# Kernel optimization log

Hardware: AMD Instinct MI355X
Metric: run time of the kernel (lower is better)

## Reference

```python
import jax, jax.numpy as jnp
import numpy as np

N_NODES = 50000
EPS = 1e-5


def sage_conv_max(x, src, dst, W_l, b_l, W_r):
    # PyG SAGEConv(aggr='max'): out = lin_l(max_j x_j) + lin_r(x_i)
    msg = x[src]                                   # [E, d] gather
    agg = jnp.full((x.shape[0], x.shape[1]), -jnp.inf, dtype=x.dtype)
    agg = agg.at[dst].max(msg)                     # scatter-max over edges
    agg = jnp.where(jnp.isneginf(agg), 0.0, agg)   # isolated nodes -> 0 (PyG convention)
    return agg @ W_l.T + b_l + x @ W_r.T


def batch_norm(x, gamma, beta):
    mean = jnp.mean(x, axis=0)
    var = jnp.var(x, axis=0)
    return (x - mean) * jax.lax.rsqrt(var + EPS) * gamma + beta


def setup_inputs() -> dict:
    key = jax.random.key(0)
    ks = jax.random.split(key, 10)
    d_in, d_h, d_out = 128, 128, 32
    s = lambda fan: 1.0 / np.sqrt(fan)
    return {
        "x": jax.random.normal(ks[0], (N_NODES, d_in), dtype=jnp.float32),
        "edge_index": jax.random.randint(ks[1], (2, 800000), 0, N_NODES, dtype=jnp.int32),
        "W_l1": jax.random.uniform(ks[2], (d_h, d_in), jnp.float32, -s(d_in), s(d_in)),
        "b_l1": jnp.zeros((d_h,), jnp.float32),
        "W_r1": jax.random.uniform(ks[3], (d_h, d_in), jnp.float32, -s(d_in), s(d_in)),
        "gamma1": jnp.ones((d_h,), jnp.float32),
        "beta1": jnp.zeros((d_h,), jnp.float32),
        "W_l2": jax.random.uniform(ks[4], (d_out, d_h), jnp.float32, -s(d_h), s(d_h)),
        "b_l2": jnp.zeros((d_out,), jnp.float32),
        "W_r2": jax.random.uniform(ks[5], (d_out, d_h), jnp.float32, -s(d_h), s(d_h)),
    }


def reference(x, edge_index, W_l1, b_l1, W_r1, gamma1, beta1, W_l2, b_l2, W_r2):
    src, dst = edge_index[0], edge_index[1]
    h = sage_conv_max(x, src, dst, W_l1, b_l1, W_r1)
    h = batch_norm(h, gamma1, beta1)
    h = jax.nn.relu(h)
    # dropout is identity at inference
    return sage_conv_max(h, src, dst, W_l2, b_l2, W_r2)
```

## Files before the change

### kernel.cpp

```cpp
#include <hip/hip_runtime.h>
#include <math.h>
#include <float.h>

#define N_NODES 50000
#define N_EDGES 800000
#define NB 392
#define EB 2048
#define NBUCK 196
#define BSH 8
#define CAP 36
#define SEGC 4864
#define CELLS_PER_BUCKET (NB * CAP)

typedef __attribute__((ext_vector_type(8))) short bf16x8;
typedef __attribute__((ext_vector_type(4))) float f32x4;

static __device__ __forceinline__ unsigned short f2bf(float f) {
  unsigned int u = __float_as_uint(f);
  u = (u + 0x7fff + ((u >> 16) & 1)) >> 16;
  return (unsigned short)u;
}

__global__ __launch_bounds__(256) void setup_kernel(
    const int* __restrict__ src, const int* __restrict__ dst,
    unsigned int* __restrict__ pairs, int* __restrict__ counts,
    const float* __restrict__ x, const float* __restrict__ Wl1,
    const float* __restrict__ Wr1, const float* __restrict__ Wl2,
    const float* __restrict__ Wr2, unsigned int* __restrict__ x_bf,
    unsigned short* __restrict__ Wcat1, unsigned short* __restrict__ Wcat2,
    float* __restrict__ gsums) {
  const int b = blockIdx.x, tid = threadIdx.x;
  if (b < NB) {
    __shared__ int cur[NBUCK];
    if (tid < NBUCK) cur[tid] = 0;
    __syncthreads();
#pragma unroll
    for (int it = 0; it < EB / 256; ++it) {
      int e = b * EB + it * 256 + tid;
      if (e < N_EDGES) {
        int d = dst[e];
        int bk = d >> BSH;
        int p = atomicAdd(&cur[bk], 1);
        if (p < CAP)
          pairs[(size_t)(bk * NB + b) * CAP + p] =
              (unsigned)src[e] | ((unsigned)(d & 255) << 16);
      }
    }
    __syncthreads();
    if (tid < NBUCK) {
      int c = cur[tid];
      counts[tid * NB + b] = c > CAP ? CAP : c;
    }
  } else if (b < NB + 6250) {
    int i = (b - NB) * 256 + tid;
    float4 v = ((const float4*)x)[i];
    uint2 o;
    o.x = (unsigned int)f2bf(v.x) | ((unsigned int)f2bf(v.y) << 16);
    o.y = (unsigned int)f2bf(v.z) | ((unsigned int)f2bf(v.w) << 16);
    ((uint2*)x_bf)[i] = o;
  } else if (b < NB + 6410) {
    int i = (b - NB - 6250) * 256 + tid;
    if (i < 32768) {
      int n = i >> 8, k = i & 255;
      float w = (k < 128) ? Wl1[n * 128 + k] : Wr1[n * 128 + (k - 128)];
      Wcat1[i] = f2bf(w);
    } else if (i < 40960) {
      int j = i - 32768;
      int n = j >> 8, k = j & 255;
      float w = (k < 128) ? Wl2[n * 128 + k] : Wr2[n * 128 + (k - 128)];
      Wcat2[j] = f2bf(w);
    }
  } else {
#pragma unroll
    for (int i = 0; i < 8; ++i) gsums[i * 256 + tid] = 0.f;
  }
}

__global__ __launch_bounds__(1024) void bucket_sort(const unsigned int* __restrict__ pairs,
                                                    const int* __restrict__ counts,
                                                    unsigned int* __restrict__ rowinfo,
                                                    int* __restrict__ elist) {
  __shared__ int hist[256], cpos[256], cnt[NB];
  __shared__ int wsum[4];
  const int b = blockIdx.x, tid = threadIdx.x;
  const size_t s0 = (size_t)b * CELLS_PER_BUCKET;
  if (tid < 256) hist[tid] = 0;
  if (tid < NB) cnt[tid] = counts[b * NB + tid];
  __syncthreads();
  for (int p = tid; p < CELLS_PER_BUCKET; p += 1024) {
    int c = p / CAP, s = p - c * CAP;
    if (s < cnt[c]) {
      unsigned int pr = pairs[s0 + p];
      atomicAdd(&hist[(pr >> 16) & 255], 1);
    }
  }
  __syncthreads();
  int incl = 0, h = 0;
  if (tid < 256) {
    const int l = tid & 63;
    h = hist[tid];
    incl = h;
#pragma unroll
    for (int off = 1; off < 64; off <<= 1) {
      int t = __shfl_up(incl, off, 64);
      if (l >= off) incl += t;
    }
    if (l == 63) wsum[tid >> 6] = incl;
  }
  __syncthreads();
  if (tid < 64) {
    int v = (tid < 4) ? wsum[tid] : 0;
#pragma unroll
    for (int off = 1; off < 4; off <<= 1) {
      int t = __shfl_up(v, off, 64);
      if (tid >= off) v += t;
    }
    if (tid < 4) wsum[tid] = v;
  }
  __syncthreads();
  if (tid < 256) {
    const int w = tid >> 6;
    int tot = incl + ((w > 0) ? wsum[w - 1] : 0);
    int excl = tot - h;
    cpos[tid] = excl;
    int node = (b << BSH) + tid;
    if (node < N_NODES)
      rowinfo[node] = (unsigned)(b * SEGC + excl) | ((unsigned)h << 20);
  }
  __syncthreads();
  for (int p = tid; p < CELLS_PER_BUCKET; p += 1024) {
    int c = p / CAP, s = p - c * CAP;
    if (s < cnt[c]) {
      unsigned int pr = pairs[s0 + p];
      int loc = atomicAdd(&cpos[(pr >> 16) & 255], 1);
      elist[b * SEGC + loc] = (int)(pr & 0xffffu);
    }
  }
}

template <bool BN>
__global__ __launch_bounds__(256) void agg_max_bf16(const uint4* __restrict__ feat4,
                                                    const unsigned int* __restrict__ rowinfo,
                                                    const int* __restrict__ elist,
                                                    const float* __restrict__ gsums,
                                                    const float* __restrict__ gamma,
                                                    const float* __restrict__ beta,
                                                    uint4* __restrict__ out4) {
  __shared__ float s_scale[128], s_shift[128];
  if (BN) {
    int t = threadIdx.x;
    if (t < 128) {
      float sm = 0.f, sq = 0.f;
#pragma unroll
      for (int r = 0; r < 8; ++r) {
        sm += gsums[r * 256 + t];
        sq += gsums[r * 256 + 128 + t];
      }
      const float inv = 1.f / (float)N_NODES;
      float mean = sm * inv;
      float var = sq * inv - mean * mean;
      float sc = gamma[t] * rsqrtf(var + 1e-5f);
      s_scale[t] = sc;
      s_shift[t] = beta[t] - mean * sc;
    }
    __syncthreads();
  }

  int node = blockIdx.x * 4 + (threadIdx.x >> 6);
  int lane = threadIdx.x & 63;
  int eslot = lane >> 4;
  int fq = lane & 15;
  unsigned int info = rowinfo[node];
  int e0 = (int)(info & 0xFFFFFu);
  int deg = (int)(info >> 20);
  int e1 = e0 + deg;
  float m[8];
#pragma unroll
  for (int j = 0; j < 8; ++j) m[j] = -FLT_MAX;

  if (deg > 0) {
    const int last = e1 - 1;
    for (int base = e0; base < e1; base += 16) {
      int idx[4];
#pragma unroll
      for (int q = 0; q < 4; ++q) {
        int e = base + q * 4 + eslot;
        if (e > last) e = last;
        idx[q] = elist[e];
      }
      uint4 v[4];
#pragma unroll
      for (int q = 0; q < 4; ++q) v[q] = feat4[(size_t)idx[q] * 16 + fq];
#pragma unroll
      for (int q = 0; q < 4; ++q) {
        const unsigned int* pv = (const unsigned int*)&v[q];
#pragma unroll
        for (int c = 0; c < 4; ++c) {
          m[2 * c]     = fmaxf(m[2 * c],     __uint_as_float(pv[c] << 16));
          m[2 * c + 1] = fmaxf(m[2 * c + 1], __uint_as_float(pv[c] & 0xffff0000u));
        }
      }
    }
  }

#pragma unroll
  for (int j = 0; j < 8; ++j) {
    m[j] = fmaxf(m[j], __shfl_xor(m[j], 16, 64));
    m[j] = fmaxf(m[j], __shfl_xor(m[j], 32, 64));
  }
  if (eslot == 0) {
    if (deg == 0) {
#pragma unroll
      for (int j = 0; j < 8; ++j) m[j] = 0.f;
    } else if (BN) {
#pragma unroll
      for (int j = 0; j < 8; ++j) {
        int col = fq * 8 + j;
        m[j] = fmaxf(m[j] * s_scale[col] + s_shift[col], 0.f);
      }
    }
    uint4 o;
    o.x = (unsigned)f2bf(m[0]) | ((unsigned)f2bf(m[1]) << 16);
    o.y = (unsigned)f2bf(m[2]) | ((unsigned)f2bf(m[3]) << 16);
    o.z = (unsigned)f2bf(m[4]) | ((unsigned)f2bf(m[5]) << 16);
    o.w = (unsigned)f2bf(m[6]) | ((unsigned)f2bf(m[7]) << 16);
    out4[(size_t)node * 16 + fq] = o;
  }
}

#define ASTR 264

template <int NT, bool BF16OUT, bool STATS, bool BNIN>
__global__ __launch_bounds__(256) void gemm_mfma(
    const unsigned short* __restrict__ Aa, const unsigned short* __restrict__ Ab,
    const unsigned short* __restrict__ Wcat, const float* __restrict__ bias,
    unsigned short* __restrict__ outb, float* __restrict__ outf,
    float* __restrict__ gsums, const float* __restrict__ gamma,
    const float* __restrict__ beta, int N) {
  __shared__ unsigned short Alds[128 * ASTR];
  __shared__ float s_sum[128], s_sq[128];
  __shared__ float s_scale[128], s_shift[128];
  const int tid = threadIdx.x;
  const int rowBase = blockIdx.x * 128;

  if (STATS && tid < 128) { s_sum[tid] = 0.f; s_sq[tid] = 0.f; }
  if (BNIN) {
    if (tid < 128) {
      float sm = 0.f, sq = 0.f;
#pragma unroll
      for (int r = 0; r < 8; ++r) {
        sm += gsums[r * 256 + tid];
        sq += gsums[r * 256 + 128 + tid];
      }
      const float inv = 1.f / (float)N_NODES;
      float mean = sm * inv;
      float var = sq * inv - mean * mean;
      float sc = gamma[tid] * rsqrtf(var + 1e-5f);
      s_scale[tid] = sc;
      s_shift[tid] = beta[tid] - mean * sc;
    }
    __syncthreads();
  }

#pragma unroll
  for (int it = 0; it < 16; ++it) {
    int f = tid + it * 256;
    int r = f >> 5;
    int seg = f & 31;
    int n = rowBase + r;
    if (n >= N) n = N - 1;
    const unsigned short* src = (seg < 16)
        ? (Aa + (size_t)n * 128 + seg * 8)
        : (Ab + (size_t)n * 128 + (seg - 16) * 8);
    int4 d = *(const int4*)src;
    if (BNIN && seg >= 16) {
      int kb = (seg - 16) * 8;
      unsigned int* dp = (unsigned int*)&d;
#pragma unroll
      for (int c = 0; c < 4; ++c) {
        int k0 = kb + 2 * c;
        float lo = __uint_as_float(dp[c] << 16);
        float hi = __uint_as_float(dp[c] & 0xffff0000u);
        lo = fmaxf(lo * s_scale[k0] + s_shift[k0], 0.f);
        hi = fmaxf(hi * s_scale[k0 + 1] + s_shift[k0 + 1], 0.f);
        dp[c] = (unsigned)f2bf(lo) | ((unsigned)f2bf(hi) << 16);
      }
    }
    *(int4*)(&Alds[r * ASTR + seg * 8]) = d;
  }
  __syncthreads();

  const int wv = tid >> 6;
  const int lane = tid & 63;
  const int ln15 = lane & 15;
  const int quad = lane >> 4;
  const int m0 = wv * 32;

  f32x4 acc[2][NT] = {};

#pragma unroll
  for (int ks = 0; ks < 8; ++ks) {
    const int k0 = ks * 32;
    bf16x8 a0 = *(const bf16x8*)(&Alds[(m0 + ln15) * ASTR + k0 + quad * 8]);
    bf16x8 a1 = *(const bf16x8*)(&Alds[(m0 + 16 + ln15) * ASTR + k0 + quad * 8]);
#pragma unroll
    for (int nt = 0; nt < NT; ++nt) {
      bf16x8 b = *(const bf16x8*)(Wcat + (size_t)(nt * 16 + ln15) * 256 + k0 + quad * 8);
      acc[0][nt] = __builtin_amdgcn_mfma_f32_16x16x32_bf16(a0, b, acc[0][nt], 0, 0, 0);
      acc[1][nt] = __builtin_amdgcn_mfma_f32_16x16x32_bf16(a1, b, acc[1][nt], 0, 0, 0);
    }
  }

  const int ldo = NT * 16;
#pragma unroll
  for (int nt = 0; nt < NT; ++nt) {
    int col = nt * 16 + ln15;
    float bv = bias[col];
    float psum = 0.f, psq = 0.f;
#pragma unroll
    for (int mt = 0; mt < 2; ++mt) {
#pragma unroll
      for (int i = 0; i < 4; ++i) {
        int r = rowBase + m0 + mt * 16 + quad * 4 + i;
        if (r < N) {
          float val = acc[mt][nt][i] + bv;
          if (STATS) { psum += val; psq += val * val; }
          if (BF16OUT)
            outb[(size_t)r * ldo + col] = f2bf(val);
          else
            outf[(size_t)r * ldo + col] = val;
        }
      }
    }
    if (STATS) {
      atomicAdd(&s_sum[col], psum);
      atomicAdd(&s_sq[col], psq);
    }
  }
  if (STATS) {
    __syncthreads();
    if (tid < 128) {
      int rep = blockIdx.x & 7;
      atomicAdd(&gsums[rep * 256 + tid], s_sum[tid]);
      atomicAdd(&gsums[rep * 256 + 128 + tid], s_sq[tid]);
    }
  }
}

extern "C" void kernel_launch(void* const* d_in, const int* in_sizes, int n_in,
                              void* d_out, int out_size, void* d_ws, size_t ws_size,
                              hipStream_t stream) {
  (void)in_sizes; (void)n_in; (void)out_size; (void)ws_size;
  const float* x     = (const float*)d_in[0];
  const int*   eidx  = (const int*)d_in[1];
  const float* W_l1  = (const float*)d_in[2];
  const float* b_l1  = (const float*)d_in[3];
  const float* W_r1  = (const float*)d_in[4];
  const float* gamma = (const float*)d_in[5];
  const float* beta  = (const float*)d_in[6];
  const float* W_l2  = (const float*)d_in[7];
  const float* b_l2  = (const float*)d_in[8];
  const float* W_r2  = (const float*)d_in[9];
  const int* srcp = eidx;
  const int* dstp = eidx + N_EDGES;
  float* out = (float*)d_out;

  int* wsi = (int*)d_ws;
  float* gsums   = (float*)wsi;
  unsigned int* rowinfo = (unsigned int*)(wsi + 2048);
  int*   counts  = wsi + 52224;
  int*   elist   = wsi + 129056;
  unsigned int* pairs   = (unsigned int*)(wsi + 1082400);
  unsigned int* x_bf    = (unsigned int*)(wsi + 3848352);
  unsigned int* agg_bf  = (unsigned int*)(wsi + 7048352);
  unsigned int* h_bf    = (unsigned int*)(wsi + 10248352);
  unsigned short* Wcat1 = (unsigned short*)(wsi + 13448352);
  unsigned short* Wcat2 = (unsigned short*)(wsi + 13464736);

  setup_kernel<<<dim3(NB + 6410 + 1), 256, 0, stream>>>(
      srcp, dstp, pairs, counts, x, W_l1, W_r1, W_l2, W_r2, x_bf, Wcat1, Wcat2, gsums);

  bucket_sort<<<dim3(NBUCK), 1024, 0, stream>>>(pairs, counts, rowinfo, elist);

  agg_max_bf16<false><<<dim3(N_NODES / 4), 256, 0, stream>>>(
      (const uint4*)x_bf, rowinfo, elist, nullptr, nullptr, nullptr, (uint4*)agg_bf);
  gemm_mfma<8, true, true, false><<<dim3(391), 256, 0, stream>>>(
      (const unsigned short*)agg_bf, (const unsigned short*)x_bf, Wcat1, b_l1,
      (unsigned short*)h_bf, nullptr, gsums, nullptr, nullptr, N_NODES);

  agg_max_bf16<true><<<dim3(N_NODES / 4), 256, 0, stream>>>(
      (const uint4*)h_bf, rowinfo, elist, gsums, gamma, beta, (uint4*)agg_bf);
  gemm_mfma<2, false, false, true><<<dim3(391), 256, 0, stream>>>(
      (const unsigned short*)agg_bf, (const unsigned short*)h_bf, Wcat2, b_l2,
      nullptr, out, gsums, gamma, beta, N_NODES);
}
```

Before: 215.7 us.

## Split max-aggregation into feature slices and fold conversions into sort kernel

The gather-max kernel now processes one 32-feature slice per block across four slice passes. Each thread loads one 4-byte word per edge instead of 16 bytes, so each pass touches a smaller feature window, which is meant to improve cache locality on random neighbor gathers. The edge scatter is moved into its own kernel, and the x/weight bf16 conversions and gsums zeroing are moved from it into the bucket-sort launch so they run alongside the sort. The cost is more blocks, narrower loads, and repeated elist and rowinfo reads for every slice.

```diff
diff --git a/kernel.cpp b/kernel.cpp
--- a/kernel.cpp
+++ b/kernel.cpp
@@ -3,6 +3,7 @@
 #include <float.h>
 
 #define N_NODES 50000
+#define N_PAD 50176
 #define N_EDGES 800000
 #define NB 392
 #define EB 2048
@@ -11,6 +12,9 @@
 #define CAP 36
 #define SEGC 4864
 #define CELLS_PER_BUCKET (NB * CAP)
+#define GB (N_PAD / 4)
+#define XC_BLKS 1563
+#define WC_BLKS 40
 
 typedef __attribute__((ext_vector_type(8))) short bf16x8;
 typedef __attribute__((ext_vector_type(4))) float f32x4;
@@ -21,68 +25,71 @@
   return (unsigned short)u;
 }
 
-__global__ __launch_bounds__(256) void setup_kernel(
+__global__ __launch_bounds__(512) void scatter_kernel(
     const int* __restrict__ src, const int* __restrict__ dst,
-    unsigned int* __restrict__ pairs, int* __restrict__ counts,
+    unsigned int* __restrict__ pairs, int* __restrict__ counts) {
+  const int b = blockIdx.x, tid = threadIdx.x;
+  __shared__ int cur[NBUCK];
+  if (tid < NBUCK) cur[tid] = 0;
+  __syncthreads();
+#pragma unroll
+  for (int it = 0; it < EB / 512; ++it) {
+    int e = b * EB + it * 512 + tid;
+    if (e < N_EDGES) {
+      int d = dst[e];
+      int bk = d >> BSH;
+      int p = atomicAdd(&cur[bk], 1);
+      if (p < CAP)
+        pairs[(size_t)(bk * NB + b) * CAP + p] =
+            (unsigned)src[e] | ((unsigned)(d & 255) << 16);
+    }
+  }
+  __syncthreads();
+  if (tid < NBUCK) {
+    int c = cur[tid];
+    counts[tid * NB + b] = c > CAP ? CAP : c;
+  }
+}
+
+__global__ __launch_bounds__(1024) void sort_conv_kernel(
+    const unsigned int* __restrict__ pairs, const int* __restrict__ counts,
+    unsigned int* __restrict__ rowinfo, int* __restrict__ elist,
     const float* __restrict__ x, const float* __restrict__ Wl1,
     const float* __restrict__ Wr1, const float* __restrict__ Wl2,
     const float* __restrict__ Wr2, unsigned int* __restrict__ x_bf,
     unsigned short* __restrict__ Wcat1, unsigned short* __restrict__ Wcat2,
     float* __restrict__ gsums) {
   const int b = blockIdx.x, tid = threadIdx.x;
-  if (b < NB) {
-    __shared__ int cur[NBUCK];
-    if (tid < NBUCK) cur[tid] = 0;
-    __syncthreads();
-#pragma unroll
-    for (int it = 0; it < EB / 256; ++it) {
-      int e = b * EB + it * 256 + tid;
-      if (e < N_EDGES) {
-        int d = dst[e];
-        int bk = d >> BSH;
-        int p = atomicAdd(&cur[bk], 1);
-        if (p < CAP)
-          pairs[(size_t)(bk * NB + b) * CAP + p] =
-              (unsigned)src[e] | ((unsigned)(d & 255) << 16);
-      }
-    }
-    __syncthreads();
-    if (tid < NBUCK) {
-      int c = cur[tid];
-      counts[tid * NB + b] = c > CAP ? CAP : c;
-    }
-  } else if (b < NB + 6250) {
-    int i = (b - NB) * 256 + tid;
-    float4 v = ((const float4*)x)[i];
-    uint2 o;
-    o.x = (unsigned int)f2bf(v.x) | ((unsigned int)f2bf(v.y) << 16);
-    o.y = (unsigned int)f2bf(v.z) | ((unsigned int)f2bf(v.w) << 16);
-    ((uint2*)x_bf)[i] = o;
-  } else if (b < NB + 6410) {
-    int i = (b - NB - 6250) * 256 + tid;
-    if (i < 32768) {
-      int n = i >> 8, k = i & 255;
-      float w = (k < 128) ? Wl1[n * 128 + k] : Wr1[n * 128 + (k - 128)];
-      Wcat1[i] = f2bf(w);
-    } else if (i < 40960) {
-      int j = i - 32768;
-      int n = j >> 8, k = j & 255;
-      float w = (k < 128) ? Wl2[n * 128 + k] : Wr2[n * 128 + (k - 128)];
-      Wcat2[j] = f2bf(w);
-    }
-  } else {
-#pragma unroll
-    for (int i = 0; i < 8; ++i) gsums[i * 256 + tid] = 0.f;
-  }
-}
-
-__global__ __launch_bounds__(1024) void bucket_sort(const unsigned int* __restrict__ pairs,
-                                                    const int* __restrict__ counts,
-                                                    unsigned int* __restrict__ rowinfo,
-                                                    int* __restrict__ elist) {
+  if (b >= NBUCK) {
+    if (b < NBUCK + XC_BLKS) {
+      int i = (b - NBUCK) * 1024 + tid;
+      if (i < 1600000) {
+        float4 v = ((const float4*)x)[i];
+        uint2 o;
+        o.x = (unsigned int)f2bf(v.x) | ((unsigned int)f2bf(v.y) << 16);
+        o.y = (unsigned int)f2bf(v.z) | ((unsigned int)f2bf(v.w) << 16);
+        ((uint2*)x_bf)[i] = o;
+      }
+    } else if (b < NBUCK + XC_BLKS + WC_BLKS) {
+      int i = (b - NBUCK - XC_BLKS) * 1024 + tid;
+      if (i < 32768) {
+        int n = i >> 8, k = i & 255;
+        float w = (k < 128) ? Wl1[n * 128 + k] : Wr1[n * 128 + (k - 128)];
+        Wcat1[i] = f2bf(w);
+      } else if (i < 40960) {
+        int j = i - 32768;
+        int n = j >> 8, k = j & 255;
+        float w = (k < 128) ? Wl2[n * 128 + k] : Wr2[n * 128 + (k - 128)];
+        Wcat2[j] = f2bf(w);
+      }
+    } else {
+      gsums[tid] = 0.f;
+      gsums[tid + 1024] = 0.f;
+    }
+    return;
+  }
   __shared__ int hist[256], cpos[256], cnt[NB];
   __shared__ int wsum[4];
-  const int b = blockIdx.x, tid = threadIdx.x;
   const size_t s0 = (size_t)b * CELLS_PER_BUCKET;
   if (tid < 256) hist[tid] = 0;
   if (tid < NB) cnt[tid] = counts[b * NB + tid];
@@ -139,92 +146,80 @@
 }
 
 template <bool BN>
-__global__ __launch_bounds__(256) void agg_max_bf16(const uint4* __restrict__ feat4,
-                                                    const unsigned int* __restrict__ rowinfo,
-                                                    const int* __restrict__ elist,
-                                                    const float* __restrict__ gsums,
-                                                    const float* __restrict__ gamma,
-                                                    const float* __restrict__ beta,
-                                                    uint4* __restrict__ out4) {
-  __shared__ float s_scale[128], s_shift[128];
+__global__ __launch_bounds__(256) void gather_slice(
+    const unsigned int* __restrict__ feat,
+    const unsigned int* __restrict__ rowinfo,
+    const int* __restrict__ elist,
+    const float* __restrict__ gsums,
+    const float* __restrict__ gamma, const float* __restrict__ beta,
+    unsigned int* __restrict__ out) {
+  __shared__ float s_scale[32], s_shift[32];
+  const int bid = blockIdx.x;
+  const int slice = bid / GB;
+  const int nb = bid - slice * GB;
+  const int tid = threadIdx.x;
   if (BN) {
-    int t = threadIdx.x;
-    if (t < 128) {
+    if (tid < 32) {
+      int f = slice * 32 + tid;
       float sm = 0.f, sq = 0.f;
 #pragma unroll
       for (int r = 0; r < 8; ++r) {
-        sm += gsums[r * 256 + t];
-        sq += gsums[r * 256 + 128 + t];
+        sm += gsums[r * 256 + f];
+        sq += gsums[r * 256 + 128 + f];
       }
       const float inv = 1.f / (float)N_NODES;
       float mean = sm * inv;
       float var = sq * inv - mean * mean;
-      float sc = gamma[t] * rsqrtf(var + 1e-5f);
-      s_scale[t] = sc;
-      s_shift[t] = beta[t] - mean * sc;
+      float sc = gamma[f] * rsqrtf(var + 1e-5f);
+      s_scale[tid] = sc;
+      s_shift[tid] = beta[f] - mean * sc;
     }
     __syncthreads();
   }
-
-  int node = blockIdx.x * 4 + (threadIdx.x >> 6);
-  int lane = threadIdx.x & 63;
-  int eslot = lane >> 4;
-  int fq = lane & 15;
+  int node = nb * 4 + (tid >> 6);
+  if (node >= N_NODES) node = N_NODES - 1;
+  const int lane = tid & 63;
+  const int eslot = lane >> 4;
+  const int fq = lane & 15;
   unsigned int info = rowinfo[node];
   int e0 = (int)(info & 0xFFFFFu);
   int deg = (int)(info >> 20);
   int e1 = e0 + deg;
-  float m[8];
-#pragma unroll
-  for (int j = 0; j < 8; ++j) m[j] = -FLT_MAX;
-
+  float m0 = -FLT_MAX, m1 = -FLT_MAX;
+  const unsigned int* fs = feat + slice * 16 + fq;
   if (deg > 0) {
     const int last = e1 - 1;
-    for (int base = e0; base < e1; base += 16) {
-      int idx[4];
-#pragma unroll
-      for (int q = 0; q < 4; ++q) {
+    for (int base = e0; base < e1; base += 8) {
+      int idx[2];
+#pragma unroll
+      for (int q = 0; q < 2; ++q) {
         int e = base + q * 4 + eslot;
         if (e > last) e = last;
         idx[q] = elist[e];
       }
-      uint4 v[4];
-#pragma unroll
-      for (int q = 0; q < 4; ++q) v[q] = feat4[(size_t)idx[q] * 16 + fq];
-#pragma unroll
-      for (int q = 0; q < 4; ++q) {
-        const unsigned int* pv = (const unsigned int*)&v[q];
-#pragma unroll
-        for (int c = 0; c < 4; ++c) {
-          m[2 * c]     = fmaxf(m[2 * c],     __uint_as_float(pv[c] << 16));
-          m[2 * c + 1] = fmaxf(m[2 * c + 1], __uint_as_float(pv[c] & 0xffff0000u));
-        }
-      }
-    }
-  }
-
-#pragma unroll
-  for (int j = 0; j < 8; ++j) {
-    m[j] = fmaxf(m[j], __shfl_xor(m[j], 16, 64));
-    m[j] = fmaxf(m[j], __shfl_xor(m[j], 32, 64));
-  }
+      unsigned int v[2];
+#pragma unroll
+      for (int q = 0; q < 2; ++q) v[q] = fs[(size_t)idx[q] * 64];
+#pragma unroll
+      for (int q = 0; q < 2; ++q) {
+        m0 = fmaxf(m0, __uint_as_float(v[q] << 16));
+        m1 = fmaxf(m1, __uint_as_float(v[q] & 0xffff0000u));
+      }
+    }
+  }
+  m0 = fmaxf(m0, __shfl_xor(m0, 16, 64));
+  m0 = fmaxf(m0, __shfl_xor(m0, 32, 64));
+  m1 = fmaxf(m1, __shfl_xor(m1, 16, 64));
+  m1 = fmaxf(m1, __shfl_xor(m1, 32, 64));
   if (eslot == 0) {
     if (deg == 0) {
-#pragma unroll
-      for (int j = 0; j < 8; ++j) m[j] = 0.f;
+      m0 = 0.f; m1 = 0.f;
     } else if (BN) {
-#pragma unroll
-      for (int j = 0; j < 8; ++j) {
-        int col = fq * 8 + j;
-        m[j] = fmaxf(m[j] * s_scale[col] + s_shift[col], 0.f);
-      }
-    }
-    uint4 o;
-    o.x = (unsigned)f2bf(m[0]) | ((unsigned)f2bf(m[1]) << 16);
-    o.y = (unsigned)f2bf(m[2]) | ((unsigned)f2bf(m[3]) << 16);
-    o.z = (unsigned)f2bf(m[4]) | ((unsigned)f2bf(m[5]) << 16);
-    o.w = (unsigned)f2bf(m[6]) | ((unsigned)f2bf(m[7]) << 16);
-    out4[(size_t)node * 16 + fq] = o;
+      m0 = fmaxf(m0 * s_scale[2 * fq] + s_shift[2 * fq], 0.f);
+      m1 = fmaxf(m1 * s_scale[2 * fq + 1] + s_shift[2 * fq + 1], 0.f);
+    }
+    out[(size_t)node * 64 + slice * 16 + fq] =
+        (unsigned)f2bf(m0) | ((unsigned)f2bf(m1) << 16);
   }
 }
 
@@ -377,19 +372,20 @@
   unsigned short* Wcat1 = (unsigned short*)(wsi + 13448352);
   unsigned short* Wcat2 = (unsigned short*)(wsi + 13464736);
 
-  setup_kernel<<<dim3(NB + 6410 + 1), 256, 0, stream>>>(
-      srcp, dstp, pairs, counts, x, W_l1, W_r1, W_l2, W_r2, x_bf, Wcat1, Wcat2, gsums);
-
-  bucket_sort<<<dim3(NBUCK), 1024, 0, stream>>>(pairs, counts, rowinfo, elist);
-
-  agg_max_bf16<false><<<dim3(N_NODES / 4), 256, 0, stream>>>(
-      (const uint4*)x_bf, rowinfo, elist, nullptr, nullptr, nullptr, (uint4*)agg_bf);
+  scatter_kernel<<<dim3(NB), 512, 0, stream>>>(srcp, dstp, pairs, counts);
+
+  sort_conv_kernel<<<dim3(NBUCK + XC_BLKS + WC_BLKS + 1), 1024, 0, stream>>>(
+      pairs, counts, rowinfo, elist, x, W_l1, W_r1, W_l2, W_r2,
+      x_bf, Wcat1, Wcat2, gsums);
+
+  gather_slice<false><<<dim3(4 * GB), 256, 0, stream>>>(
+      x_bf, rowinfo, elist, nullptr, nullptr, nullptr, agg_bf);
   gemm_mfma<8, true, true, false><<<dim3(391), 256, 0, stream>>>(
       (const unsigned short*)agg_bf, (const unsigned short*)x_bf, Wcat1, b_l1,
       (unsigned short*)h_bf, nullptr, gsums, nullptr, nullptr, N_NODES);
 
-  agg_max_bf16<true><<<dim3(N_NODES / 4), 256, 0, stream>>>(
-      (const uint4*)h_bf, rowinfo, elist, gsums, gamma, beta, (uint4*)agg_bf);
+  gather_slice<true><<<dim3(4 * GB), 256, 0, stream>>>(
+      h_bf, rowinfo, elist, gsums, gamma, beta, agg_bf);
   gemm_mfma<2, false, false, true><<<dim3(391), 256, 0, stream>>>(
       (const unsigned short*)agg_bf, (const unsigned short*)h_bf, Wcat2, b_l2,
       nullptr, out, gsums, gamma, beta, N_NODES);
```

Measured after the change: 304.5 us. 41.1% more time.

## Load GEMM A operands directly from global, drop LDS staging and halve row tile

Applied to the files above, without the earlier changes.

The GEMM kernels no longer stage the 128-row A tile in LDS. Each wave now loads its 16-row A fragments straight from global memory, with BN+ReLU applied in registers for the second layer. The block covers 64 rows instead of 128 and the grid doubles to 784 blocks, which frees the large LDS allocation, raises occupancy and removes the staging sync. In exchange, each B fragment is reused across only one M tile instead of two, and the global A loads are strided per lane rather than fully coalesced.

```diff
diff --git a/kernel.cpp b/kernel.cpp
--- a/kernel.cpp
+++ b/kernel.cpp
@@ -228,8 +228,6 @@
   }
 }
 
-#define ASTR 264
-
 template <int NT, bool BF16OUT, bool STATS, bool BNIN>
 __global__ __launch_bounds__(256) void gemm_mfma(
     const unsigned short* __restrict__ Aa, const unsigned short* __restrict__ Ab,
@@ -237,56 +235,25 @@
     unsigned short* __restrict__ outb, float* __restrict__ outf,
     float* __restrict__ gsums, const float* __restrict__ gamma,
     const float* __restrict__ beta, int N) {
-  __shared__ unsigned short Alds[128 * ASTR];
   __shared__ float s_sum[128], s_sq[128];
   __shared__ float s_scale[128], s_shift[128];
   const int tid = threadIdx.x;
-  const int rowBase = blockIdx.x * 128;
+  const int rowBase = blockIdx.x * 64;
 
   if (STATS && tid < 128) { s_sum[tid] = 0.f; s_sq[tid] = 0.f; }
-  if (BNIN) {
-    if (tid < 128) {
-      float sm = 0.f, sq = 0.f;
-#pragma unroll
-      for (int r = 0; r < 8; ++r) {
-        sm += gsums[r * 256 + tid];
-        sq += gsums[r * 256 + 128 + tid];
-      }
-      const float inv = 1.f / (float)N_NODES;
-      float mean = sm * inv;
-      float var = sq * inv - mean * mean;
-      float sc = gamma[tid] * rsqrtf(var + 1e-5f);
-      s_scale[tid] = sc;
-      s_shift[tid] = beta[tid] - mean * sc;
-    }
-    __syncthreads();
-  }
-
-#pragma unroll
-  for (int it = 0; it < 16; ++it) {
-    int f = tid + it * 256;
-    int r = f >> 5;
-    int seg = f & 31;
-    int n = rowBase + r;
-    if (n >= N) n = N - 1;
-    const unsigned short* src = (seg < 16)
-        ? (Aa + (size_t)n * 128 + seg * 8)
-        : (Ab + (size_t)n * 128 + (seg - 16) * 8);
-    int4 d = *(const int4*)src;
-    if (BNIN && seg >= 16) {
-      int kb = (seg - 16) * 8;
-      unsigned int* dp = (unsigned int*)&d;
-#pragma unroll
-      for (int c = 0; c < 4; ++c) {
-        int k0 = kb + 2 * c;
-        float lo = __uint_as_float(dp[c] << 16);
-        float hi = __uint_as_float(dp[c] & 0xffff0000u);
-        lo = fmaxf(lo * s_scale[k0] + s_shift[k0], 0.f);
-        hi = fmaxf(hi * s_scale[k0 + 1] + s_shift[k0 + 1], 0.f);
-        dp[c] = (unsigned)f2bf(lo) | ((unsigned)f2bf(hi) << 16);
-      }
-    }
-    *(int4*)(&Alds[r * ASTR + seg * 8]) = d;
+  if (BNIN && tid < 128) {
+    float sm = 0.f, sq = 0.f;
+#pragma unroll
+    for (int r = 0; r < 8; ++r) {
+      sm += gsums[r * 256 + tid];
+      sq += gsums[r * 256 + 128 + tid];
+    }
+    const float inv = 1.f / (float)N_NODES;
+    float mean = sm * inv;
+    float var = sq * inv - mean * mean;
+    float sc = gamma[tid] * rsqrtf(var + 1e-5f);
+    s_scale[tid] = sc;
+    s_shift[tid] = beta[tid] - mean * sc;
   }
   __syncthreads();
 
@@ -294,20 +261,38 @@
   const int lane = tid & 63;
   const int ln15 = lane & 15;
   const int quad = lane >> 4;
-  const int m0 = wv * 32;
-
-  f32x4 acc[2][NT] = {};
+  const int mrow = rowBase + wv * 16;
+  int r0 = mrow + ln15;
+  if (r0 >= N) r0 = N - 1;
+
+  f32x4 acc[NT] = {};
 
 #pragma unroll
   for (int ks = 0; ks < 8; ++ks) {
-    const int k0 = ks * 32;
-    bf16x8 a0 = *(const bf16x8*)(&Alds[(m0 + ln15) * ASTR + k0 + quad * 8]);
-    bf16x8 a1 = *(const bf16x8*)(&Alds[(m0 + 16 + ln15) * ASTR + k0 + quad * 8]);
+    const int off = ks * 32 + quad * 8;
+    bf16x8 a;
+    if (ks < 4) {
+      a = *(const bf16x8*)(Aa + (size_t)r0 * 128 + off);
+    } else {
+      const int kb = off - 128;
+      a = *(const bf16x8*)(Ab + (size_t)r0 * 128 + kb);
+      if (BNIN) {
+        unsigned int* p = (unsigned int*)&a;
+#pragma unroll
+        for (int c = 0; c < 4; ++c) {
+          int k = kb + 2 * c;
+          float lo = __uint_as_float(p[c] << 16);
+          float hi = __uint_as_float(p[c] & 0xffff0000u);
+          lo = fmaxf(lo * s_scale[k] + s_shift[k], 0.f);
+          hi = fmaxf(hi * s_scale[k + 1] + s_shift[k + 1], 0.f);
+          p[c] = (unsigned)f2bf(lo) | ((unsigned)f2bf(hi) << 16);
+        }
+      }
+    }
 #pragma unroll
     for (int nt = 0; nt < NT; ++nt) {
-      bf16x8 b = *(const bf16x8*)(Wcat + (size_t)(nt * 16 + ln15) * 256 + k0 + quad * 8);
-      acc[0][nt] = __builtin_amdgcn_mfma_f32_16x16x32_bf16(a0, b, acc[0][nt], 0, 0, 0);
-      acc[1][nt] = __builtin_amdgcn_mfma_f32_16x16x32_bf16(a1, b, acc[1][nt], 0, 0, 0);
+      bf16x8 b = *(const bf16x8*)(Wcat + (size_t)(nt * 16 + ln15) * 256 + off);
+      acc[nt] = __builtin_amdgcn_mfma_f32_16x16x32_bf16(a, b, acc[nt], 0, 0, 0);
     }
   }
 
@@ -318,18 +303,15 @@
     float bv = bias[col];
     float psum = 0.f, psq = 0.f;
 #pragma unroll
-    for (int mt = 0; mt < 2; ++mt) {
-#pragma unroll
-      for (int i = 0; i < 4; ++i) {
-        int r = rowBase + m0 + mt * 16 + quad * 4 + i;
-        if (r < N) {
-          float val = acc[mt][nt][i] + bv;
-          if (STATS) { psum += val; psq += val * val; }
-          if (BF16OUT)
-            outb[(size_t)r * ldo + col] = f2bf(val);
-          else
-            outf[(size_t)r * ldo + col] = val;
-        }
+    for (int i = 0; i < 4; ++i) {
+      int r = mrow + quad * 4 + i;
+      if (r < N) {
+        float val = acc[nt][i] + bv;
+        if (STATS) { psum += val; psq += val * val; }
+        if (BF16OUT)
+          outb[(size_t)r * ldo + col] = f2bf(val);
+        else
+          outf[(size_t)r * ldo + col] = val;
       }
     }
     if (STATS) {
@@ -384,13 +366,13 @@
 
   agg_max_bf16<false><<<dim3(N_NODES / 4), 256, 0, stream>>>(
       (const uint4*)x_bf, rowinfo, elist, nullptr, nullptr, nullptr, (uint4*)agg_bf);
-  gemm_mfma<8, true, true, false><<<dim3(391), 256, 0, stream>>>(
+  gemm_mfma<8, true, true, false><<<dim3(784), 256, 0, stream>>>(
       (const unsigned short*)agg_bf, (const unsigned short*)x_bf, Wcat1, b_l1,
       (unsigned short*)h_bf, nullptr, gsums, nullptr, nullptr, N_NODES);
 
   agg_max_bf16<true><<<dim3(N_NODES / 4), 256, 0, stream>>>(
       (const uint4*)h_bf, rowinfo, elist, gsums, gamma, beta, (uint4*)agg_bf);
-  gemm_mfma<2, false, false, true><<<dim3(391), 256, 0, stream>>>(
+  gemm_mfma<2, false, false, true><<<dim3(784), 256, 0, stream>>>(
       (const unsigned short*)agg_bf, (const unsigned short*)h_bf, Wcat2, b_l2,
       nullptr, out, gsums, gamma, beta, N_NODES);
 }
```

New measurement: 233.9 us. 1.08x slower.
